# Kernel optimization log

Measured on AMD Instinct MI355X. Metric: run time of the kernel, lower is better.

Reference implementation:

```python
import jax, jax.numpy as jnp
import numpy as np

N = 50000      # total nodes
E = 800000     # total edges (before self-loops)
B = 512        # graphs in batch
H = 4          # attention heads
D = 64         # per-head dim (hidden 256 = H*D)
F_IN = 203     # node feature dim
HID = H * D
NEG_SLOPE = 0.2  # PyG GATConv LeakyReLU default
LN_EPS = 1e-5


def setup_inputs() -> dict:
    key = jax.random.key(0)
    ks = jax.random.split(key, 24)
    g = lambda k, shape, fan: (jax.random.normal(k, shape, jnp.float32) / np.sqrt(fan))
    inp = {
        "x": jax.random.normal(ks[0], (N, F_IN), jnp.float32),
        "edge_index": jax.random.randint(ks[1], (2, E), 0, N, jnp.int64),
        "edge_weight": jax.random.uniform(ks[2], (E,), jnp.float32),
        "batch": jnp.sort(jax.random.randint(ks[3], (N,), 0, B, jnp.int64)),
        # GAT layer 1 params
        "W1": g(ks[4], (HID, F_IN), F_IN),
        "a_s1": g(ks[5], (H, D), D),
        "a_d1": g(ks[6], (H, D), D),
        "a_e1": g(ks[7], (H, D), D),
        "We1": g(ks[8], (HID, 1), 1),
        "b1": jnp.zeros((HID,), jnp.float32),
        # GAT layer 2 params
        "W2": g(ks[9], (HID, HID), HID),
        "a_s2": g(ks[10], (H, D), D),
        "a_d2": g(ks[11], (H, D), D),
        "a_e2": g(ks[12], (H, D), D),
        "We2": g(ks[13], (HID, 1), 1),
        "b2": jnp.zeros((HID,), jnp.float32),
        # LayerNorms
        "ln1_g": jnp.ones((HID,), jnp.float32),
        "ln1_b": jnp.zeros((HID,), jnp.float32),
        "ln2_g": jnp.ones((HID,), jnp.float32),
        "ln2_b": jnp.zeros((HID,), jnp.float32),
    }
    return inp


def _gat(x, src, dst, e_attr, W, a_s, a_d, a_e, We, bias, n_nodes):
    # projected node features: [N, H, D]
    xp = (x @ W.T).reshape(n_nodes, H, D)
    alpha_src = jnp.einsum('nhd,hd->nh', xp, a_s)   # [N, H]
    alpha_dst = jnp.einsum('nhd,hd->nh', xp, a_d)   # [N, H]
    ep = (e_attr @ We.T).reshape(-1, H, D)          # [E', H, D]
    alpha_edge = jnp.einsum('ehd,hd->eh', ep, a_e)  # [E', H]
    logits = jax.nn.leaky_relu(alpha_src[src] + alpha_dst[dst] + alpha_edge, NEG_SLOPE)
    # segment softmax over incoming edges per destination node
    m = jax.ops.segment_max(logits, dst, num_segments=n_nodes)
    ex = jnp.exp(logits - m[dst])
    denom = jax.ops.segment_sum(ex, dst, num_segments=n_nodes)
    alpha = ex / denom[dst]                          # [E', H]
    msg = alpha[:, :, None] * xp[src]                # [E', H, D]
    out = jax.ops.segment_sum(msg, dst, num_segments=n_nodes)
    return out.reshape(n_nodes, HID) + bias


def _ln(x, g, b):
    mu = x.mean(-1, keepdims=True)
    var = ((x - mu) ** 2).mean(-1, keepdims=True)
    return (x - mu) * jax.lax.rsqrt(var + LN_EPS) * g + b


def reference(x, edge_index, edge_weight, batch,
              W1, a_s1, a_d1, a_e1, We1, b1,
              W2, a_s2, a_d2, a_e2, We2, b2,
              ln1_g, ln1_b, ln2_g, ln2_b):
    n = x.shape[0]
    # PyG GATConv add_self_loops=True, edge_attr fill_value='mean'
    loop = jnp.arange(n)
    src = jnp.concatenate([edge_index[0], loop])
    dst = jnp.concatenate([edge_index[1], loop])
    ew = jnp.concatenate([edge_weight, jnp.full((n,), edge_weight.mean(), edge_weight.dtype)])
    e_attr = ew[:, None]  # edge_dim = 1

    h = _gat(x, src, dst, e_attr, W1, a_s1, a_d1, a_e1, We1, b1, n)
    h = jax.nn.elu(_ln(h, ln1_g, ln1_b))  # dropout omitted (eval mode)
    h = _gat(h, src, dst, e_attr, W2, a_s2, a_d2, a_e2, We2, b2, n)
    h = jax.nn.elu(_ln(h, ln2_g, ln2_b))

    # global_mean_pool
    s = jax.ops.segment_sum(h, batch, num_segments=B)
    cnt = jax.ops.segment_sum(jnp.ones((n,), h.dtype), batch, num_segments=B)
    return s / jnp.maximum(cnt, 1.0)[:, None]
```

## Files before the change

### kernel.cpp

```cpp
#include <hip/hip_runtime.h>
#include <math.h>

#define HID 256
#define NEG_SLOPE 0.2f
#define LN_EPS 1e-5f

typedef __attribute__((ext_vector_type(4))) float f32x4;
typedef __attribute__((ext_vector_type(8))) short bf16x8;
typedef __attribute__((address_space(3))) unsigned char lds_b;
typedef const __attribute__((address_space(1))) unsigned char glob_b;

__device__ __forceinline__ float bf2f_lo(unsigned int u) {
    union { unsigned int i; float f; } c; c.i = u << 16; return c.f;
}
__device__ __forceinline__ float bf2f_hi(unsigned int u) {
    union { unsigned int i; float f; } c; c.i = u & 0xffff0000u; return c.f;
}
__device__ __forceinline__ float bf2f_u(unsigned short u) {
    union { unsigned int i; float f; } c; c.i = ((unsigned int)u) << 16; return c.f;
}
__device__ __forceinline__ unsigned short f2bf(float f) {
    union { float f; unsigned int i; } c; c.f = f;
    unsigned int i = c.i;
    return (unsigned short)((i + 0x7fffu + ((i >> 16) & 1u)) >> 16);
}

__global__ __launch_bounds__(256) void sum_stage1(const float* __restrict__ w, int n, float* __restrict__ partials) {
    __shared__ float sdata[4];
    float v = 0.f;
    for (int i = blockIdx.x * 256 + threadIdx.x; i < n; i += gridDim.x * 256) v += w[i];
    for (int o = 32; o; o >>= 1) v += __shfl_xor(v, o);
    if ((threadIdx.x & 63) == 0) sdata[threadIdx.x >> 6] = v;
    __syncthreads();
    if (threadIdx.x == 0) partials[blockIdx.x] = sdata[0] + sdata[1] + sdata[2] + sdata[3];
}

__global__ __launch_bounds__(256) void sum2_coeff_kernel(const float* __restrict__ partials, float* __restrict__ sumw,
                                                         const float* __restrict__ We1, const float* __restrict__ ae1,
                                                         const float* __restrict__ We2, const float* __restrict__ ae2,
                                                         float* __restrict__ c1, float* __restrict__ c2) {
    int t = threadIdx.x;
    if (blockIdx.x == 0) {
        __shared__ float sdata[4];
        float v = partials[t];
        for (int o = 32; o; o >>= 1) v += __shfl_xor(v, o);
        if ((t & 63) == 0) sdata[t >> 6] = v;
        __syncthreads();
        if (t == 0) *sumw = sdata[0] + sdata[1] + sdata[2] + sdata[3];
    } else {
        float v1 = We1[t] * ae1[t];
        float v2 = We2[t] * ae2[t];
        for (int o = 1; o < 64; o <<= 1) { v1 += __shfl_xor(v1, o); v2 += __shfl_xor(v2, o); }
        if ((t & 63) == 0) { c1[t >> 6] = v1; c2[t >> 6] = v2; }
    }
}

__global__ __launch_bounds__(256) void hist_kernel(const int* __restrict__ ei, int E, int N, int* __restrict__ deg) {
    int e = blockIdx.x * 256 + threadIdx.x;
    if (e >= E + N) return;
    int d = (e < E) ? ei[E + e] : (e - E);
    atomicAdd(&deg[d], 1);
}

__global__ __launch_bounds__(256) void scan_reduce(const int* __restrict__ deg, int N, int* __restrict__ bsum) {
    __shared__ int sdata[4];
    int i = blockIdx.x * 256 + threadIdx.x;
    int v = (i < N) ? deg[i] : 0;
    for (int o = 32; o; o >>= 1) v += __shfl_xor(v, o);
    if ((threadIdx.x & 63) == 0) sdata[threadIdx.x >> 6] = v;
    __syncthreads();
    if (threadIdx.x == 0) bsum[blockIdx.x] = sdata[0] + sdata[1] + sdata[2] + sdata[3];
}

__global__ __launch_bounds__(256) void scan_bsums(const int* __restrict__ bsum, int NB, int* __restrict__ boff) {
    __shared__ int sm[256];
    int t = threadIdx.x;
    int v = (t < NB) ? bsum[t] : 0;
    sm[t] = v;
    __syncthreads();
    for (int o = 1; o < 256; o <<= 1) {
        int tv = (t >= o) ? sm[t - o] : 0;
        __syncthreads();
        sm[t] += tv;
        __syncthreads();
    }
    if (t < NB) boff[t] = sm[t] - v;
}

__global__ __launch_bounds__(256) void scan_apply(const int* __restrict__ deg, int N, const int* __restrict__ boff,
                                                  int* __restrict__ offs, int* __restrict__ cursor) {
    __shared__ int sm[256];
    int t = threadIdx.x;
    int i = blockIdx.x * 256 + t;
    int v = (i < N) ? deg[i] : 0;
    sm[t] = v;
    __syncthreads();
    for (int o = 1; o < 256; o <<= 1) {
        int tv = (t >= o) ? sm[t - o] : 0;
        __syncthreads();
        sm[t] += tv;
        __syncthreads();
    }
    if (i < N) {
        int e = boff[blockIdx.x] + sm[t] - v;
        offs[i] = e; cursor[i] = e;
        if (i == N - 1) offs[N] = boff[blockIdx.x] + sm[t];
    }
}

__global__ __launch_bounds__(256) void scatter_eid(const int* __restrict__ ei, int E, int N,
                                                   int* __restrict__ cursor, int* __restrict__ csr_eid) {
    int e = blockIdx.x * 256 + threadIdx.x;
    if (e >= E + N) return;
    int d = (e < E) ? ei[E + e] : (e - E);
    int pos = atomicAdd(&cursor[d], 1);
    csr_eid[pos] = e;
}

__global__ __launch_bounds__(256) void sort_gather_kernel(const int* __restrict__ offs, int* __restrict__ eid,
                                                          const int* __restrict__ ei, const float* __restrict__ ew,
                                                          const float* __restrict__ sumw, int E, int N,
                                                          int* __restrict__ csr_src, float* __restrict__ csr_w) {
    int lane = threadIdx.x & 63;
    int n = (blockIdx.x << 2) + (threadIdx.x >> 6);
    if (n >= N) return;
    int s0 = offs[n];
    int d = offs[n + 1] - s0;
    if (d <= 0) return;
    if (d <= 64) {
        int key = (lane < d) ? eid[s0 + lane] : 0x7fffffff;
        int rank = 0;
        for (int j = 0; j < d; j++) {
            int kj = __shfl(key, j);
            rank += (kj < key) ? 1 : 0;
        }
        if (lane < d) {
            int s; float wv;
            if (key < E) { s = ei[key]; wv = ew[key]; }
            else         { s = key - E; wv = *sumw / (float)E; }
            csr_src[s0 + rank] = s;
            csr_w[s0 + rank] = wv;
        }
    } else {
        if (lane == 0) {
            for (int i = s0 + 1; i < s0 + d; i++) {
                int ke = eid[i];
                int j = i - 1;
                while (j >= s0 && eid[j] > ke) { eid[j + 1] = eid[j]; j--; }
                eid[j + 1] = ke;
            }
        }
        __builtin_amdgcn_wave_barrier();
        for (int i = lane; i < d; i += 64) {
            int e = eid[s0 + i];
            int s; float wv;
            if (e < E) { s = ei[e]; wv = ew[e]; }
            else       { s = e - E; wv = *sumw / (float)E; }
            csr_src[s0 + i] = s;
            csr_w[s0 + i] = wv;
        }
    }
}

__global__ __launch_bounds__(256) void cvt_pad_kernel(const float* __restrict__ in, unsigned short* __restrict__ out, int K) {
    int r = blockIdx.x, t = threadIdx.x;
    out[(size_t)r * 256 + t] = (t < K) ? f2bf(in[(size_t)r * K + t]) : (unsigned short)0;
}

__global__ __launch_bounds__(256) void cvt_w_both(const float* __restrict__ W1, const float* __restrict__ W2,
                                                  unsigned short* __restrict__ o1, unsigned short* __restrict__ o2,
                                                  int K1) {
    int b = blockIdx.x, k = threadIdx.x;
    const float* in = (b < 256) ? W1 : W2;
    unsigned short* out = (b < 256) ? o1 : o2;
    int K = (b < 256) ? K1 : 256;
    int col = b & 255;
    float v = (k < K) ? in[(size_t)col * K + k] : 0.f;
    int ks = k >> 5, j = (k >> 3) & 3, e = k & 7;
    out[ks * 8192 + j * 2048 + ((((col << 4) ^ (j << 4))) >> 1) + e] = f2bf(v);
}

__global__ __launch_bounds__(256) void gemm_mfma(
    const unsigned short* __restrict__ A16, const unsigned short* __restrict__ Bt16, int M,
    const float* __restrict__ asf, const float* __restrict__ adf,
    unsigned short* __restrict__ C16, float* __restrict__ as_out, float* __restrict__ ad_out)
{
    __shared__ __align__(16) unsigned short Bsl[4 * 256 * 8];
    int t = threadIdx.x;
    int lane = t & 63, w = t >> 6;
    int row0 = blockIdx.x << 5;
    int kg = lane >> 4, fr = lane & 15;

    int ar0 = row0 + fr;      if (ar0 >= M) ar0 = 0;
    int ar1 = row0 + 16 + fr; if (ar1 >= M) ar1 = 0;
    const unsigned short* ap0 = A16 + (size_t)ar0 * 256 + (kg << 3);
    const unsigned short* ap1 = A16 + (size_t)ar1 * 256 + (kg << 3);

    f32x4 acc[2][4];
#pragma unroll
    for (int i = 0; i < 2; i++)
#pragma unroll
        for (int j = 0; j < 4; j++) acc[i][j] = (f32x4){0.f, 0.f, 0.f, 0.f};

    for (int ks = 0; ks < 8; ks++) {
#pragma unroll
        for (int j = 0; j < 4; j++) {
            __builtin_amdgcn_global_load_lds(
                (glob_b*)(Bt16 + (size_t)ks * 8192 + j * 2048 + t * 8),
                (lds_b*)((char*)Bsl + j * 4096 + t * 16),
                16, 0, 0);
        }
        bf16x8 a0 = *(const bf16x8*)(ap0 + (ks << 5));
        bf16x8 a1 = *(const bf16x8*)(ap1 + (ks << 5));
        __syncthreads();
#pragma unroll
        for (int nf = 0; nf < 4; nf++) {
            int col = (w << 6) + (nf << 4) + fr;
            bf16x8 bv = *(const bf16x8*)((const char*)Bsl + (kg << 12) + (((col << 4)) ^ (kg << 4)));
            acc[0][nf] = __builtin_amdgcn_mfma_f32_16x16x32_bf16(a0, bv, acc[0][nf], 0, 0, 0);
            acc[1][nf] = __builtin_amdgcn_mfma_f32_16x16x32_bf16(a1, bv, acc[1][nf], 0, 0, 0);
        }
        __syncthreads();
    }

#pragma unroll
    for (int mf = 0; mf < 2; mf++)
#pragma unroll
        for (int j = 0; j < 4; j++) {
            int gr = row0 + mf * 16 + kg * 4 + j;
            if (gr < M) {
#pragma unroll
                for (int nf = 0; nf < 4; nf++)
                    C16[(size_t)gr * 256 + (w << 6) + (nf << 4) + fr] = f2bf(acc[mf][nf][j]);
            }
        }
    float asv[4], adv[4];
#pragma unroll
    for (int nf = 0; nf < 4; nf++) {
        int col = (w << 6) + (nf << 4) + fr;
        asv[nf] = asf[col]; adv[nf] = adf[col];
    }
#pragma unroll
    for (int mf = 0; mf < 2; mf++)
#pragma unroll
        for (int j = 0; j < 4; j++) {
            float ps = acc[mf][0][j] * asv[0] + acc[mf][1][j] * asv[1] + acc[mf][2][j] * asv[2] + acc[mf][3][j] * asv[3];
            float pd = acc[mf][0][j] * adv[0] + acc[mf][1][j] * adv[1] + acc[mf][2][j] * adv[2] + acc[mf][3][j] * adv[3];
#pragma unroll
            for (int o = 1; o < 16; o <<= 1) { ps += __shfl_xor(ps, o); pd += __shfl_xor(pd, o); }
            if (fr == 0) {
                int gr = row0 + mf * 16 + kg * 4 + j;
                if (gr < M) {
                    as_out[gr * 4 + w] = ps;
                    ad_out[gr * 4 + w] = pd;
                }
            }
        }
}

#define ACC8(u, q) do { \
    acc0 += (q) * bf2f_lo((u).x); acc1 += (q) * bf2f_hi((u).x); \
    acc2 += (q) * bf2f_lo((u).y); acc3 += (q) * bf2f_hi((u).y); \
    acc4 += (q) * bf2f_lo((u).z); acc5 += (q) * bf2f_hi((u).z); \
    acc6 += (q) * bf2f_lo((u).w); acc7 += (q) * bf2f_hi((u).w); } while (0)

__global__ __launch_bounds__(256) void gat_kernel(
    const unsigned short* __restrict__ xp16, const int* __restrict__ offs,
    const int* __restrict__ csr_src, const float* __restrict__ csr_w,
    const float* __restrict__ as_, const float* __restrict__ ad_,
    const float* __restrict__ cvec, const float* __restrict__ bias,
    const float* __restrict__ ln_g, const float* __restrict__ ln_b,
    int N, unsigned short* __restrict__ out16) {
    __shared__ float p_lds[4][256];
    __shared__ int   s_lds[4][64];
    int lane = threadIdx.x & 63;
    int wid = threadIdx.x >> 6;
    int n = (blockIdx.x << 2) + wid;
    if (n >= N) return;
    int start = offs[n], end = offs[n + 1];
    int e0 = lane >> 5;
    int colb = lane & 31;
    int hq2 = colb >> 3;
    const unsigned short* xbase = xp16 + (size_t)colb * 8;
    float4 adv = *(const float4*)(ad_ + (size_t)n * 4);
    float c0 = cvec[0], c1 = cvec[1], c2 = cvec[2], c3 = cvec[3];
    float m = -INFINITY, dn = 0.f;
    float acc0 = 0, acc1 = 0, acc2 = 0, acc3 = 0, acc4 = 0, acc5 = 0, acc6 = 0, acc7 = 0;

    for (int base = start; base < end; base += 64) {
        int idx = base + lane;
        bool act = idx < end;
        int s = act ? csr_src[idx] : 0;
        float w = act ? csr_w[idx] : 0.f;
        float4 av = *(const float4*)(as_ + (size_t)s * 4);
        float l0 = av.x + adv.x + w * c0; l0 = l0 >= 0.f ? l0 : NEG_SLOPE * l0;
        float l1 = av.y + adv.y + w * c1; l1 = l1 >= 0.f ? l1 : NEG_SLOPE * l1;
        float l2 = av.z + adv.z + w * c2; l2 = l2 >= 0.f ? l2 : NEG_SLOPE * l2;
        float l3 = av.w + adv.w + w * c3; l3 = l3 >= 0.f ? l3 : NEG_SLOPE * l3;
        float lm = fmaxf(fmaxf(l0, l1), fmaxf(l2, l3));
        if (!act) lm = -INFINITY;
        for (int o = 32; o; o >>= 1) lm = fmaxf(lm, __shfl_xor(lm, o));
        float nm = fmaxf(m, lm);
        float sc = __expf(m - nm);
        m = nm;
        dn *= sc;
        acc0 *= sc; acc1 *= sc; acc2 *= sc; acc3 *= sc;
        acc4 *= sc; acc5 *= sc; acc6 *= sc; acc7 *= sc;
        float p0 = act ? __expf(l0 - m) : 0.f;
        float p1 = act ? __expf(l1 - m) : 0.f;
        float p2 = act ? __expf(l2 - m) : 0.f;
        float p3 = act ? __expf(l3 - m) : 0.f;
        float4 pv = { p0, p1, p2, p3 };
        *(float4*)&p_lds[wid][lane << 2] = pv;
        s_lds[wid][lane] = s;
        int cnt = end - base; if (cnt > 64) cnt = 64;
        int k = 0;
        for (; k + 8 <= cnt; k += 8) {
            int i0 = k + e0, i1 = k + 2 + e0, i2 = k + 4 + e0, i3 = k + 6 + e0;
            int s0 = s_lds[wid][i0], s1 = s_lds[wid][i1], s2 = s_lds[wid][i2], s3 = s_lds[wid][i3];
            uint4 u0 = *(const uint4*)(xbase + (size_t)s0 * 256);
            uint4 u1 = *(const uint4*)(xbase + (size_t)s1 * 256);
            uint4 u2 = *(const uint4*)(xbase + (size_t)s2 * 256);
            uint4 u3 = *(const uint4*)(xbase + (size_t)s3 * 256);
            float q0 = p_lds[wid][(i0 << 2) + hq2];
            float q1 = p_lds[wid][(i1 << 2) + hq2];
            float q2 = p_lds[wid][(i2 << 2) + hq2];
            float q3 = p_lds[wid][(i3 << 2) + hq2];
            dn += q0 + q1 + q2 + q3;
            ACC8(u0, q0); ACC8(u1, q1); ACC8(u2, q2); ACC8(u3, q3);
        }
        for (; k < cnt; k += 2) {
            int i = k + e0;
            bool v = i < cnt;
            int si = s_lds[wid][v ? i : 0];
            float qi = v ? p_lds[wid][(i << 2) + hq2] : 0.f;
            uint4 u = *(const uint4*)(xbase + (size_t)si * 256);
            dn += qi;
            ACC8(u, qi);
        }
    }
    acc0 += __shfl_xor(acc0, 32); acc1 += __shfl_xor(acc1, 32);
    acc2 += __shfl_xor(acc2, 32); acc3 += __shfl_xor(acc3, 32);
    acc4 += __shfl_xor(acc4, 32); acc5 += __shfl_xor(acc5, 32);
    acc6 += __shfl_xor(acc6, 32); acc7 += __shfl_xor(acc7, 32);
    dn += __shfl_xor(dn, 32);
    float inv = 1.f / dn;
    int cb8 = colb << 3;
    float4 bA = *(const float4*)(bias + cb8);
    float4 bB = *(const float4*)(bias + cb8 + 4);
    float o0 = acc0 * inv + bA.x, o1 = acc1 * inv + bA.y, o2 = acc2 * inv + bA.z, o3 = acc3 * inv + bA.w;
    float o4 = acc4 * inv + bB.x, o5 = acc5 * inv + bB.y, o6 = acc6 * inv + bB.z, o7 = acc7 * inv + bB.w;
    float part = ((o0 + o1) + (o2 + o3)) + ((o4 + o5) + (o6 + o7));
    for (int o = 16; o; o >>= 1) part += __shfl_xor(part, o);
    float mu = part * (1.f / 256.f);
    float d0 = o0 - mu, d1 = o1 - mu, d2 = o2 - mu, d3 = o3 - mu;
    float d4 = o4 - mu, d5 = o5 - mu, d6 = o6 - mu, d7 = o7 - mu;
    float vpart = ((d0 * d0 + d1 * d1) + (d2 * d2 + d3 * d3)) + ((d4 * d4 + d5 * d5) + (d6 * d6 + d7 * d7));
    for (int o = 16; o; o >>= 1) vpart += __shfl_xor(vpart, o);
    float rstd = rsqrtf(vpart * (1.f / 256.f) + LN_EPS);
    float4 gA = *(const float4*)(ln_g + cb8), gB = *(const float4*)(ln_g + cb8 + 4);
    float4 eA = *(const float4*)(ln_b + cb8), eB = *(const float4*)(ln_b + cb8 + 4);
    float y0 = d0 * rstd * gA.x + eA.x; y0 = y0 > 0.f ? y0 : __expf(y0) - 1.f;
    float y1 = d1 * rstd * gA.y + eA.y; y1 = y1 > 0.f ? y1 : __expf(y1) - 1.f;
    float y2 = d2 * rstd * gA.z + eA.z; y2 = y2 > 0.f ? y2 : __expf(y2) - 1.f;
    float y3 = d3 * rstd * gA.w + eA.w; y3 = y3 > 0.f ? y3 : __expf(y3) - 1.f;
    float y4 = d4 * rstd * gB.x + eB.x; y4 = y4 > 0.f ? y4 : __expf(y4) - 1.f;
    float y5 = d5 * rstd * gB.y + eB.y; y5 = y5 > 0.f ? y5 : __expf(y5) - 1.f;
    float y6 = d6 * rstd * gB.z + eB.z; y6 = y6 > 0.f ? y6 : __expf(y6) - 1.f;
    float y7 = d7 * rstd * gB.w + eB.w; y7 = y7 > 0.f ? y7 : __expf(y7) - 1.f;
    if (lane < 32) {
        uint4 ov;
        ov.x = ((unsigned int)f2bf(y1) << 16) | f2bf(y0);
        ov.y = ((unsigned int)f2bf(y3) << 16) | f2bf(y2);
        ov.z = ((unsigned int)f2bf(y5) << 16) | f2bf(y4);
        ov.w = ((unsigned int)f2bf(y7) << 16) | f2bf(y6);
        *(uint4*)(out16 + (size_t)n * HID + cb8) = ov;
    }
}

__device__ __forceinline__ int lower_bound_i(const int* a, int n, int key) {
    int lo = 0, hi = n;
    while (lo < hi) { int mid = (lo + hi) >> 1; if (a[mid] < key) lo = mid + 1; else hi = mid; }
    return lo;
}

__global__ __launch_bounds__(256) void pool_kernel(const unsigned short* __restrict__ h, const int* __restrict__ batch,
                                                   int N, float* __restrict__ out) {
    int b = blockIdx.x;
    int lo = lower_bound_i(batch, N, b);
    int hi = lower_bound_i(batch, N, b + 1);
    float a0 = 0.f, a1 = 0.f, a2 = 0.f, a3 = 0.f;
    int n = lo;
    for (; n + 4 <= hi; n += 4) {
        a0 += bf2f_u(h[(size_t)(n + 0) * HID + threadIdx.x]);
        a1 += bf2f_u(h[(size_t)(n + 1) * HID + threadIdx.x]);
        a2 += bf2f_u(h[(size_t)(n + 2) * HID + threadIdx.x]);
        a3 += bf2f_u(h[(size_t)(n + 3) * HID + threadIdx.x]);
    }
    for (; n < hi; n++) a0 += bf2f_u(h[(size_t)n * HID + threadIdx.x]);
    float acc = (a0 + a1) + (a2 + a3);
    out[(size_t)b * HID + threadIdx.x] = acc / fmaxf((float)(hi - lo), 1.f);
}

extern "C" void kernel_launch(void* const* d_in, const int* in_sizes, int n_in,
                              void* d_out, int out_size, void* d_ws, size_t ws_size,
                              hipStream_t stream) {
    const float* x    = (const float*)d_in[0];
    const int*   ei   = (const int*)d_in[1];
    const float* ew   = (const float*)d_in[2];
    const int*   batch= (const int*)d_in[3];
    const float* W1   = (const float*)d_in[4];
    const float* as1  = (const float*)d_in[5];
    const float* ad1  = (const float*)d_in[6];
    const float* ae1  = (const float*)d_in[7];
    const float* We1  = (const float*)d_in[8];
    const float* b1   = (const float*)d_in[9];
    const float* W2   = (const float*)d_in[10];
    const float* as2  = (const float*)d_in[11];
    const float* ad2  = (const float*)d_in[12];
    const float* ae2  = (const float*)d_in[13];
    const float* We2  = (const float*)d_in[14];
    const float* b2   = (const float*)d_in[15];
    const float* ln1g = (const float*)d_in[16];
    const float* ln1b = (const float*)d_in[17];
    const float* ln2g = (const float*)d_in[18];
    const float* ln2b = (const float*)d_in[19];

    int N = in_sizes[3];
    int E = in_sizes[2];
    int FIN = in_sizes[0] / N;
    int EN = E + N;
    int B = out_size / HID;
    float* outp = (float*)d_out;
    int NB = (N + 255) / 256;

    char* ws = (char*)d_ws;
    size_t off = 0;
    auto alloc = [&](size_t bytes) { void* p = ws + off; off = (off + bytes + 255) & ~(size_t)255; return p; };
    float* sumw    = (float*)alloc(4);
    int*   deg     = (int*)  alloc((size_t)N * 4);
    size_t zero_bytes = 256 + (size_t)N * 4;
    float* partials= (float*)alloc(256 * 4);
    int*   bsum    = (int*)  alloc(256 * 4);
    int*   boff    = (int*)  alloc(256 * 4);
    int*   offs    = (int*)  alloc((size_t)(N + 1) * 4);
    int*   cursor  = (int*)  alloc((size_t)N * 4);
    int*   csr_eid = (int*)  alloc((size_t)EN * 4);
    int*   csr_src = (int*)  alloc((size_t)EN * 4);
    float* csr_w   = (float*)alloc((size_t)EN * 4);
    float* asb     = (float*)alloc((size_t)N * 4 * 4);
    float* adb     = (float*)alloc((size_t)N * 4 * 4);
    float* cc      = (float*)alloc(64);
    unsigned short* w1_16 = (unsigned short*)alloc((size_t)HID * HID * 2);
    unsigned short* w2_16 = (unsigned short*)alloc((size_t)HID * HID * 2);
    unsigned short* x16   = (unsigned short*)alloc((size_t)N * HID * 2);
    unsigned short* xp16  = (unsigned short*)alloc((size_t)N * HID * 2);
    (void)ws_size; (void)n_in;

    (void)hipMemsetAsync(d_ws, 0, zero_bytes, stream);
    sum_stage1<<<256, 256, 0, stream>>>(ew, E, partials);
    sum2_coeff_kernel<<<2, 256, 0, stream>>>(partials, sumw, We1, ae1, We2, ae2, cc, cc + 4);
    hist_kernel<<<(EN + 255) / 256, 256, 0, stream>>>(ei, E, N, deg);
    scan_reduce<<<NB, 256, 0, stream>>>(deg, N, bsum);
    scan_bsums<<<1, 256, 0, stream>>>(bsum, NB, boff);
    scan_apply<<<NB, 256, 0, stream>>>(deg, N, boff, offs, cursor);
    scatter_eid<<<(EN + 255) / 256, 256, 0, stream>>>(ei, E, N, cursor, csr_eid);
    sort_gather_kernel<<<(N + 3) / 4, 256, 0, stream>>>(offs, csr_eid, ei, ew, sumw, E, N, csr_src, csr_w);

    cvt_w_both<<<512, 256, 0, stream>>>(W1, W2, w1_16, w2_16, FIN);
    cvt_pad_kernel<<<N, 256, 0, stream>>>(x, x16, FIN);

    int MB = (N + 31) / 32;
    gemm_mfma<<<MB, 256, 0, stream>>>(x16, w1_16, N, as1, ad1, xp16, asb, adb);
    gat_kernel<<<(N + 3) / 4, 256, 0, stream>>>(xp16, offs, csr_src, csr_w, asb, adb, cc, b1, ln1g, ln1b, N, x16);
    gemm_mfma<<<MB, 256, 0, stream>>>(x16, w2_16, N, as2, ad2, xp16, asb, adb);
    gat_kernel<<<(N + 3) / 4, 256, 0, stream>>>(xp16, offs, csr_src, csr_w, asb, adb, cc + 4, b2, ln2g, ln2b, N, x16);
    pool_kernel<<<B, 256, 0, stream>>>(x16, batch, N, outp);
}
```

Before: 369.1 us.

## Merge preprocessing kernels into fewer launches via block-range dispatch

Independent preprocessing stages are combined into multi-role kernels, with the block index selecting the role. The weight-sum and degree histogram share one launch, scan-reduce shares one with the coefficient setup, and the block-offset scan is recomputed redundantly inside each scan-apply block. Edge scatter runs alongside the weight and feature bf16 conversions, and the first GEMM runs alongside the CSR sort/gather. This cuts launch count and serialization gaps and lets independent work overlap, at the cost of mixed-role blocks and higher shared-memory use in the merged kernels.

```diff
diff --git a/kernel.cpp b/kernel.cpp
--- a/kernel.cpp
+++ b/kernel.cpp
@@ -25,22 +25,43 @@
     return (unsigned short)((i + 0x7fffu + ((i >> 16) & 1u)) >> 16);
 }
 
-__global__ __launch_bounds__(256) void sum_stage1(const float* __restrict__ w, int n, float* __restrict__ partials) {
-    __shared__ float sdata[4];
-    float v = 0.f;
-    for (int i = blockIdx.x * 256 + threadIdx.x; i < n; i += gridDim.x * 256) v += w[i];
-    for (int o = 32; o; o >>= 1) v += __shfl_xor(v, o);
-    if ((threadIdx.x & 63) == 0) sdata[threadIdx.x >> 6] = v;
-    __syncthreads();
-    if (threadIdx.x == 0) partials[blockIdx.x] = sdata[0] + sdata[1] + sdata[2] + sdata[3];
-}
-
-__global__ __launch_bounds__(256) void sum2_coeff_kernel(const float* __restrict__ partials, float* __restrict__ sumw,
-                                                         const float* __restrict__ We1, const float* __restrict__ ae1,
-                                                         const float* __restrict__ We2, const float* __restrict__ ae2,
-                                                         float* __restrict__ c1, float* __restrict__ c2) {
+__global__ __launch_bounds__(256) void k_sum_hist(const float* __restrict__ ew, int E,
+                                                  const int* __restrict__ ei, int N,
+                                                  float* __restrict__ partials, int* __restrict__ deg) {
     int t = threadIdx.x;
-    if (blockIdx.x == 0) {
+    if (blockIdx.x < 256) {
+        __shared__ float sdata[4];
+        float v = 0.f;
+        for (int i = blockIdx.x * 256 + t; i < E; i += 65536) v += ew[i];
+        for (int o = 32; o; o >>= 1) v += __shfl_xor(v, o);
+        if ((t & 63) == 0) sdata[t >> 6] = v;
+        __syncthreads();
+        if (t == 0) partials[blockIdx.x] = sdata[0] + sdata[1] + sdata[2] + sdata[3];
+    } else {
+        int e = (blockIdx.x - 256) * 256 + t;
+        if (e >= E + N) return;
+        int d = (e < E) ? ei[E + e] : (e - E);
+        atomicAdd(&deg[d], 1);
+    }
+}
+
+__global__ __launch_bounds__(256) void k_scanred_coeff(const int* __restrict__ deg, int N, int NB,
+                                                       int* __restrict__ bsum,
+                                                       const float* __restrict__ partials, float* __restrict__ sumw,
+                                                       const float* __restrict__ We1, const float* __restrict__ ae1,
+                                                       const float* __restrict__ We2, const float* __restrict__ ae2,
+                                                       float* __restrict__ c1, float* __restrict__ c2) {
+    int t = threadIdx.x;
+    int b = blockIdx.x;
+    if (b < NB) {
+        __shared__ int sdata[4];
+        int i = b * 256 + t;
+        int v = (i < N) ? deg[i] : 0;
+        for (int o = 32; o; o >>= 1) v += __shfl_xor(v, o);
+        if ((t & 63) == 0) sdata[t >> 6] = v;
+        __syncthreads();
+        if (t == 0) bsum[b] = sdata[0] + sdata[1] + sdata[2] + sdata[3];
+    } else if (b == NB) {
         __shared__ float sdata[4];
         float v = partials[t];
         for (int o = 32; o; o >>= 1) v += __shfl_xor(v, o);
@@ -55,74 +76,147 @@
     }
 }
 
-__global__ __launch_bounds__(256) void hist_kernel(const int* __restrict__ ei, int E, int N, int* __restrict__ deg) {
-    int e = blockIdx.x * 256 + threadIdx.x;
-    if (e >= E + N) return;
-    int d = (e < E) ? ei[E + e] : (e - E);
-    atomicAdd(&deg[d], 1);
-}
-
-__global__ __launch_bounds__(256) void scan_reduce(const int* __restrict__ deg, int N, int* __restrict__ bsum) {
-    __shared__ int sdata[4];
-    int i = blockIdx.x * 256 + threadIdx.x;
+__global__ __launch_bounds__(256) void k_scan_apply(const int* __restrict__ deg, int N, int NB,
+                                                    const int* __restrict__ bsum,
+                                                    int* __restrict__ offs, int* __restrict__ cursor) {
+    __shared__ int sm[256];
+    __shared__ int sb[256];
+    int t = threadIdx.x;
+    int i = blockIdx.x * 256 + t;
     int v = (i < N) ? deg[i] : 0;
-    for (int o = 32; o; o >>= 1) v += __shfl_xor(v, o);
-    if ((threadIdx.x & 63) == 0) sdata[threadIdx.x >> 6] = v;
-    __syncthreads();
-    if (threadIdx.x == 0) bsum[blockIdx.x] = sdata[0] + sdata[1] + sdata[2] + sdata[3];
-}
-
-__global__ __launch_bounds__(256) void scan_bsums(const int* __restrict__ bsum, int NB, int* __restrict__ boff) {
-    __shared__ int sm[256];
-    int t = threadIdx.x;
-    int v = (t < NB) ? bsum[t] : 0;
+    int vb = (t < NB) ? bsum[t] : 0;
     sm[t] = v;
+    sb[t] = vb;
     __syncthreads();
     for (int o = 1; o < 256; o <<= 1) {
         int tv = (t >= o) ? sm[t - o] : 0;
+        int tb = (t >= o) ? sb[t - o] : 0;
         __syncthreads();
         sm[t] += tv;
-        __syncthreads();
-    }
-    if (t < NB) boff[t] = sm[t] - v;
-}
-
-__global__ __launch_bounds__(256) void scan_apply(const int* __restrict__ deg, int N, const int* __restrict__ boff,
-                                                  int* __restrict__ offs, int* __restrict__ cursor) {
-    __shared__ int sm[256];
+        sb[t] += tb;
+        __syncthreads();
+    }
+    int myb = bsum[blockIdx.x];
+    int boff = sb[blockIdx.x] - myb;
+    if (i < N) {
+        int e = boff + sm[t] - v;
+        offs[i] = e; cursor[i] = e;
+        if (i == N - 1) offs[N] = boff + sm[t];
+    }
+}
+
+__global__ __launch_bounds__(256) void k_scatter_cvt(const int* __restrict__ ei, int E, int N, int NS,
+                                                     int* __restrict__ cursor, int* __restrict__ csr_eid,
+                                                     const float* __restrict__ W1, const float* __restrict__ W2,
+                                                     unsigned short* __restrict__ o1, unsigned short* __restrict__ o2, int K1,
+                                                     const float* __restrict__ x, unsigned short* __restrict__ x16, int FIN) {
     int t = threadIdx.x;
-    int i = blockIdx.x * 256 + t;
-    int v = (i < N) ? deg[i] : 0;
-    sm[t] = v;
-    __syncthreads();
-    for (int o = 1; o < 256; o <<= 1) {
-        int tv = (t >= o) ? sm[t - o] : 0;
-        __syncthreads();
-        sm[t] += tv;
-        __syncthreads();
-    }
-    if (i < N) {
-        int e = boff[blockIdx.x] + sm[t] - v;
-        offs[i] = e; cursor[i] = e;
-        if (i == N - 1) offs[N] = boff[blockIdx.x] + sm[t];
-    }
-}
-
-__global__ __launch_bounds__(256) void scatter_eid(const int* __restrict__ ei, int E, int N,
-                                                   int* __restrict__ cursor, int* __restrict__ csr_eid) {
-    int e = blockIdx.x * 256 + threadIdx.x;
-    if (e >= E + N) return;
-    int d = (e < E) ? ei[E + e] : (e - E);
-    int pos = atomicAdd(&cursor[d], 1);
-    csr_eid[pos] = e;
-}
-
-__global__ __launch_bounds__(256) void sort_gather_kernel(const int* __restrict__ offs, int* __restrict__ eid,
-                                                          const int* __restrict__ ei, const float* __restrict__ ew,
-                                                          const float* __restrict__ sumw, int E, int N,
-                                                          int* __restrict__ csr_src, float* __restrict__ csr_w) {
+    int b = blockIdx.x;
+    if (b < NS) {
+        int e = b * 256 + t;
+        if (e >= E + N) return;
+        int d = (e < E) ? ei[E + e] : (e - E);
+        int pos = atomicAdd(&cursor[d], 1);
+        csr_eid[pos] = e;
+    } else if (b < NS + 512) {
+        int wb = b - NS;
+        const float* in = (wb < 256) ? W1 : W2;
+        unsigned short* out = (wb < 256) ? o1 : o2;
+        int K = (wb < 256) ? K1 : 256;
+        int col = wb & 255;
+        float v = (t < K) ? in[(size_t)col * K + t] : 0.f;
+        int ks = t >> 5, j = (t >> 3) & 3, e = t & 7;
+        out[ks * 8192 + j * 2048 + ((((col << 4) ^ (j << 4))) >> 1) + e] = f2bf(v);
+    } else {
+        int r = b - NS - 512;
+        x16[(size_t)r * 256 + t] = (t < FIN) ? f2bf(x[(size_t)r * FIN + t]) : (unsigned short)0;
+    }
+}
+
+__device__ __forceinline__ void gemm_dev(int bid,
+    const unsigned short* __restrict__ A16, const unsigned short* __restrict__ Bt16, int M,
+    const float* __restrict__ asf, const float* __restrict__ adf,
+    unsigned short* __restrict__ C16, float* __restrict__ as_out, float* __restrict__ ad_out)
+{
+    __shared__ __align__(16) unsigned short Bsl[4 * 256 * 8];
+    int t = threadIdx.x;
+    int lane = t & 63, w = t >> 6;
+    int row0 = bid << 5;
+    int kg = lane >> 4, fr = lane & 15;
+
+    int ar0 = row0 + fr;      if (ar0 >= M) ar0 = 0;
+    int ar1 = row0 + 16 + fr; if (ar1 >= M) ar1 = 0;
+    const unsigned short* ap0 = A16 + (size_t)ar0 * 256 + (kg << 3);
+    const unsigned short* ap1 = A16 + (size_t)ar1 * 256 + (kg << 3);
+
+    f32x4 acc[2][4];
+#pragma unroll
+    for (int i = 0; i < 2; i++)
+#pragma unroll
+        for (int j = 0; j < 4; j++) acc[i][j] = (f32x4){0.f, 0.f, 0.f, 0.f};
+
+    for (int ks = 0; ks < 8; ks++) {
+#pragma unroll
+        for (int j = 0; j < 4; j++) {
+            __builtin_amdgcn_global_load_lds(
+                (glob_b*)(Bt16 + (size_t)ks * 8192 + j * 2048 + t * 8),
+                (lds_b*)((char*)Bsl + j * 4096 + t * 16),
+                16, 0, 0);
+        }
+        bf16x8 a0 = *(const bf16x8*)(ap0 + (ks << 5));
+        bf16x8 a1 = *(const bf16x8*)(ap1 + (ks << 5));
+        __syncthreads();
+#pragma unroll
+        for (int nf = 0; nf < 4; nf++) {
+            int col = (w << 6) + (nf << 4) + fr;
+            bf16x8 bv = *(const bf16x8*)((const char*)Bsl + (kg << 12) + (((col << 4)) ^ (kg << 4)));
+            acc[0][nf] = __builtin_amdgcn_mfma_f32_16x16x32_bf16(a0, bv, acc[0][nf], 0, 0, 0);
+            acc[1][nf] = __builtin_amdgcn_mfma_f32_16x16x32_bf16(a1, bv, acc[1][nf], 0, 0, 0);
+        }
+        __syncthreads();
+    }
+
+#pragma unroll
+    for (int mf = 0; mf < 2; mf++)
+#pragma unroll
+        for (int j = 0; j < 4; j++) {
+            int gr = row0 + mf * 16 + kg * 4 + j;
+            if (gr < M) {
+#pragma unroll
+                for (int nf = 0; nf < 4; nf++)
+                    C16[(size_t)gr * 256 + (w << 6) + (nf << 4) + fr] = f2bf(acc[mf][nf][j]);
+            }
+        }
+    float asv[4], adv[4];
+#pragma unroll
+    for (int nf = 0; nf < 4; nf++) {
+        int col = (w << 6) + (nf << 4) + fr;
+        asv[nf] = asf[col]; adv[nf] = adf[col];
+    }
+#pragma unroll
+    for (int mf = 0; mf < 2; mf++)
+#pragma unroll
+        for (int j = 0; j < 4; j++) {
+            float ps = acc[mf][0][j] * asv[0] + acc[mf][1][j] * asv[1] + acc[mf][2][j] * asv[2] + acc[mf][3][j] * asv[3];
+            float pd = acc[mf][0][j] * adv[0] + acc[mf][1][j] * adv[1] + acc[mf][2][j] * adv[2] + acc[mf][3][j] * adv[3];
+#pragma unroll
+            for (int o = 1; o < 16; o <<= 1) { ps += __shfl_xor(ps, o); pd += __shfl_xor(pd, o); }
+            if (fr == 0) {
+                int gr = row0 + mf * 16 + kg * 4 + j;
+                if (gr < M) {
+                    as_out[gr * 4 + w] = ps;
+                    ad_out[gr * 4 + w] = pd;
+                }
+            }
+        }
+}
+
+__device__ __forceinline__ void sort_gather_dev(int bid, const int* __restrict__ offs, int* __restrict__ eid,
+                                                const int* __restrict__ ei, const float* __restrict__ ew,
+                                                const float* __restrict__ sumw, int E, int N,
+                                                int* __restrict__ csr_src, float* __restrict__ csr_w) {
     int lane = threadIdx.x & 63;
-    int n = (blockIdx.x << 2) + (threadIdx.x >> 6);
+    int n = (bid << 2) + (threadIdx.x >> 6);
     if (n >= N) return;
     int s0 = offs[n];
     int d = offs[n + 1] - s0;
@@ -162,100 +256,25 @@
     }
 }
 
-__global__ __launch_bounds__(256) void cvt_pad_kernel(const float* __restrict__ in, unsigned short* __restrict__ out, int K) {
-    int r = blockIdx.x, t = threadIdx.x;
-    out[(size_t)r * 256 + t] = (t < K) ? f2bf(in[(size_t)r * K + t]) : (unsigned short)0;
-}
-
-__global__ __launch_bounds__(256) void cvt_w_both(const float* __restrict__ W1, const float* __restrict__ W2,
-                                                  unsigned short* __restrict__ o1, unsigned short* __restrict__ o2,
-                                                  int K1) {
-    int b = blockIdx.x, k = threadIdx.x;
-    const float* in = (b < 256) ? W1 : W2;
-    unsigned short* out = (b < 256) ? o1 : o2;
-    int K = (b < 256) ? K1 : 256;
-    int col = b & 255;
-    float v = (k < K) ? in[(size_t)col * K + k] : 0.f;
-    int ks = k >> 5, j = (k >> 3) & 3, e = k & 7;
-    out[ks * 8192 + j * 2048 + ((((col << 4) ^ (j << 4))) >> 1) + e] = f2bf(v);
+__global__ __launch_bounds__(256) void k_gemm_sort(int MB,
+    const unsigned short* __restrict__ A16, const unsigned short* __restrict__ Bt16, int M,
+    const float* __restrict__ asf, const float* __restrict__ adf,
+    unsigned short* __restrict__ C16, float* __restrict__ as_out, float* __restrict__ ad_out,
+    const int* __restrict__ offs, int* __restrict__ eid,
+    const int* __restrict__ ei, const float* __restrict__ ew,
+    const float* __restrict__ sumw, int E,
+    int* __restrict__ csr_src, float* __restrict__ csr_w) {
+    if ((int)blockIdx.x < MB)
+        gemm_dev(blockIdx.x, A16, Bt16, M, asf, adf, C16, as_out, ad_out);
+    else
+        sort_gather_dev(blockIdx.x - MB, offs, eid, ei, ew, sumw, E, M, csr_src, csr_w);
 }
 
 __global__ __launch_bounds__(256) void gemm_mfma(
     const unsigned short* __restrict__ A16, const unsigned short* __restrict__ Bt16, int M,
     const float* __restrict__ asf, const float* __restrict__ adf,
-    unsigned short* __restrict__ C16, float* __restrict__ as_out, float* __restrict__ ad_out)
-{
-    __shared__ __align__(16) unsigned short Bsl[4 * 256 * 8];
-    int t = threadIdx.x;
-    int lane = t & 63, w = t >> 6;
-    int row0 = blockIdx.x << 5;
-    int kg = lane >> 4, fr = lane & 15;
-
-    int ar0 = row0 + fr;      if (ar0 >= M) ar0 = 0;
-    int ar1 = row0 + 16 + fr; if (ar1 >= M) ar1 = 0;
-    const unsigned short* ap0 = A16 + (size_t)ar0 * 256 + (kg << 3);
-    const unsigned short* ap1 = A16 + (size_t)ar1 * 256 + (kg << 3);
-
-    f32x4 acc[2][4];
-#pragma unroll
-    for (int i = 0; i < 2; i++)
-#pragma unroll
-        for (int j = 0; j < 4; j++) acc[i][j] = (f32x4){0.f, 0.f, 0.f, 0.f};
-
-    for (int ks = 0; ks < 8; ks++) {
-#pragma unroll
-        for (int j = 0; j < 4; j++) {
-            __builtin_amdgcn_global_load_lds(
-                (glob_b*)(Bt16 + (size_t)ks * 8192 + j * 2048 + t * 8),
-                (lds_b*)((char*)Bsl + j * 4096 + t * 16),
-                16, 0, 0);
-        }
-        bf16x8 a0 = *(const bf16x8*)(ap0 + (ks << 5));
-        bf16x8 a1 = *(const bf16x8*)(ap1 + (ks << 5));
-        __syncthreads();
-#pragma unroll
-        for (int nf = 0; nf < 4; nf++) {
-            int col = (w << 6) + (nf << 4) + fr;
-            bf16x8 bv = *(const bf16x8*)((const char*)Bsl + (kg << 12) + (((col << 4)) ^ (kg << 4)));
-            acc[0][nf] = __builtin_amdgcn_mfma_f32_16x16x32_bf16(a0, bv, acc[0][nf], 0, 0, 0);
-            acc[1][nf] = __builtin_amdgcn_mfma_f32_16x16x32_bf16(a1, bv, acc[1][nf], 0, 0, 0);
-        }
-        __syncthreads();
-    }
-
-#pragma unroll
-    for (int mf = 0; mf < 2; mf++)
-#pragma unroll
-        for (int j = 0; j < 4; j++) {
-            int gr = row0 + mf * 16 + kg * 4 + j;
-            if (gr < M) {
-#pragma unroll
-                for (int nf = 0; nf < 4; nf++)
-                    C16[(size_t)gr * 256 + (w << 6) + (nf << 4) + fr] = f2bf(acc[mf][nf][j]);
-            }
-        }
-    float asv[4], adv[4];
-#pragma unroll
-    for (int nf = 0; nf < 4; nf++) {
-        int col = (w << 6) + (nf << 4) + fr;
-        asv[nf] = asf[col]; adv[nf] = adf[col];
-    }
-#pragma unroll
-    for (int mf = 0; mf < 2; mf++)
-#pragma unroll
-        for (int j = 0; j < 4; j++) {
-            float ps = acc[mf][0][j] * asv[0] + acc[mf][1][j] * asv[1] + acc[mf][2][j] * asv[2] + acc[mf][3][j] * asv[3];
-            float pd = acc[mf][0][j] * adv[0] + acc[mf][1][j] * adv[1] + acc[mf][2][j] * adv[2] + acc[mf][3][j] * adv[3];
-#pragma unroll
-            for (int o = 1; o < 16; o <<= 1) { ps += __shfl_xor(ps, o); pd += __shfl_xor(pd, o); }
-            if (fr == 0) {
-                int gr = row0 + mf * 16 + kg * 4 + j;
-                if (gr < M) {
-                    as_out[gr * 4 + w] = ps;
-                    ad_out[gr * 4 + w] = pd;
-                }
-            }
-        }
+    unsigned short* __restrict__ C16, float* __restrict__ as_out, float* __restrict__ ad_out) {
+    gemm_dev(blockIdx.x, A16, Bt16, M, asf, adf, C16, as_out, ad_out);
 }
 
 #define ACC8(u, q) do { \
@@ -433,6 +452,7 @@
     int B = out_size / HID;
     float* outp = (float*)d_out;
     int NB = (N + 255) / 256;
+    int NS = (EN + 255) / 256;
 
     char* ws = (char*)d_ws;
     size_t off = 0;
@@ -442,7 +462,6 @@
     size_t zero_bytes = 256 + (size_t)N * 4;
     float* partials= (float*)alloc(256 * 4);
     int*   bsum    = (int*)  alloc(256 * 4);
-    int*   boff    = (int*)  alloc(256 * 4);
     int*   offs    = (int*)  alloc((size_t)(N + 1) * 4);
     int*   cursor  = (int*)  alloc((size_t)N * 4);
     int*   csr_eid = (int*)  alloc((size_t)EN * 4);
@@ -457,21 +476,16 @@
     unsigned short* xp16  = (unsigned short*)alloc((size_t)N * HID * 2);
     (void)ws_size; (void)n_in;
 
+    int MB = (N + 31) / 32;
+
     (void)hipMemsetAsync(d_ws, 0, zero_bytes, stream);
-    sum_stage1<<<256, 256, 0, stream>>>(ew, E, partials);
-    sum2_coeff_kernel<<<2, 256, 0, stream>>>(partials, sumw, We1, ae1, We2, ae2, cc, cc + 4);
-    hist_kernel<<<(EN + 255) / 256, 256, 0, stream>>>(ei, E, N, deg);
-    scan_reduce<<<NB, 256, 0, stream>>>(deg, N, bsum);
-    scan_bsums<<<1, 256, 0, stream>>>(bsum, NB, boff);
-    scan_apply<<<NB, 256, 0, stream>>>(deg, N, boff, offs, cursor);
-    scatter_eid<<<(EN + 255) / 256, 256, 0, stream>>>(ei, E, N, cursor, csr_eid);
-    sort_gather_kernel<<<(N + 3) / 4, 256, 0, stream>>>(offs, csr_eid, ei, ew, sumw, E, N, csr_src, csr_w);
-
-    cvt_w_both<<<512, 256, 0, stream>>>(W1, W2, w1_16, w2_16, FIN);
-    cvt_pad_kernel<<<N, 256, 0, stream>>>(x, x16, FIN);
-
-    int MB = (N + 31) / 32;
-    gemm_mfma<<<MB, 256, 0, stream>>>(x16, w1_16, N, as1, ad1, xp16, asb, adb);
+    k_sum_hist<<<256 + NS, 256, 0, stream>>>(ew, E, ei, N, partials, deg);
+    k_scanred_coeff<<<NB + 2, 256, 0, stream>>>(deg, N, NB, bsum, partials, sumw, We1, ae1, We2, ae2, cc, cc + 4);
+    k_scan_apply<<<NB, 256, 0, stream>>>(deg, N, NB, bsum, offs, cursor);
+    k_scatter_cvt<<<NS + 512 + N, 256, 0, stream>>>(ei, E, N, NS, cursor, csr_eid,
+                                                    W1, W2, w1_16, w2_16, FIN, x, x16, FIN);
+    k_gemm_sort<<<MB + (N + 3) / 4, 256, 0, stream>>>(MB, x16, w1_16, N, as1, ad1, xp16, asb, adb,
+                                                      offs, csr_eid, ei, ew, sumw, E, csr_src, csr_w);
     gat_kernel<<<(N + 3) / 4, 256, 0, stream>>>(xp16, offs, csr_src, csr_w, asb, adb, cc, b1, ln1g, ln1b, N, x16);
     gemm_mfma<<<MB, 256, 0, stream>>>(x16, w2_16, N, as2, ad2, xp16, asb, adb);
     gat_kernel<<<(N + 3) / 4, 256, 0, stream>>>(xp16, offs, csr_src, csr_w, asb, adb, cc + 4, b2, ln2g, ln2b, N, x16);
```

After: 352.4 us. -4.5%, faster.
